# Performance work log

Hardware: AMD Instinct MI355X
Metric: run time of the kernel (lower is better)

## Reference

```python
import jax, jax.numpy as jnp
import numpy as np

N, R, T = 40000, 2000, 500000   # node_size, rel_size, triple_size
D, DEPTH, PROXY_N = 128, 2, 64  # node_F, depth, proxy rows
DC = D * (DEPTH + 1)            # 384


def _unique_edges(rng, n_rows, n_cols, n_edges):
    # sorted, duplicate-free edge list -> matches torch.sparse coalesce() ordering
    keys = np.unique(rng.integers(0, n_rows * n_cols, size=int(n_edges * 1.05), dtype=np.int64))[:n_edges]
    assert keys.shape[0] == n_edges
    return np.stack([keys // n_cols, keys % n_cols], axis=1)


def _init_emb(key, r, c):
    w = jax.random.normal(key, (r, c), dtype=jnp.float32)
    return w / jnp.maximum(jnp.linalg.norm(w, axis=1, keepdims=True), 1e-12)


def setup_inputs() -> dict:
    rng = np.random.default_rng(0)
    adj = jnp.asarray(_unique_edges(rng, N, N, T))                    # [T,2] (src, dst)
    idx = jnp.stack([jnp.arange(T), jnp.asarray(rng.integers(0, R, T, dtype=np.int64))], axis=1)  # [T,2]
    val = jnp.ones((T,), jnp.float32)
    ent_m = jnp.asarray(_unique_edges(rng, N, N, T))
    rel_m = jnp.asarray(_unique_edges(rng, N, R, T))
    ks = jax.random.split(jax.random.key(0), 12)
    return {
        "ent_emb": _init_emb(ks[0], N, D),
        "rel_emb": _init_emb(ks[1], R, D),
        "e_gate": _init_emb(ks[2], DC, DC),
        "e_proxy": _init_emb(ks[3], PROXY_N, DC),
        "e_bias": _init_emb(ks[4], 1, DC),
        "e_attn": jnp.stack([_init_emb(ks[5], D, 1), _init_emb(ks[6], D, 1)]),
        "r_gate": _init_emb(ks[7], DC, DC),
        "r_proxy": _init_emb(ks[8], PROXY_N, DC),
        "r_bias": _init_emb(ks[9], 1, DC),
        "r_attn": jnp.stack([_init_emb(ks[10], D, 1), _init_emb(ks[11], D, 1)]),
        "val_input": val,
        "adj_input": adj,
        "index_input": idx,
        "ent_matrix": ent_m,
        "rel_matrix": rel_m,
    }


def _l2(x):
    return x / jnp.maximum(jnp.linalg.norm(x, axis=-1, keepdims=True), 1e-12)


def _seg_softmax(v, seg, n):
    m = jax.ops.segment_max(v, seg, num_segments=n)
    e = jnp.exp(v - m[seg])
    s = jax.ops.segment_sum(e, seg, num_segments=n)
    return e / s[seg]


def _adj_agg(edges, emb, n_rows):
    # torch.sparse.softmax over rows of an all-ones adjacency, then sparse @ emb
    rows, cols = edges[:, 0], edges[:, 1]
    w = _seg_softmax(jnp.zeros(edges.shape[0], emb.dtype), rows, n_rows)
    return jax.ops.segment_sum(w[:, None] * emb[cols], rows, num_segments=n_rows)


def _graph_attention(features, rel_emb, edges, sp_idx, sp_val, attn, gate_k, proxy, bias):
    n = features.shape[0]
    t = sp_val.shape[0]
    feats = jnp.tanh(features)
    outs = [feats]
    for l in range(DEPTH):
        # sparse (T,R) @ rel_emb -> per-edge relation embedding, then L2 normalize
        rels_sum = _l2(jax.ops.segment_sum(sp_val[:, None] * rel_emb[sp_idx[:, 1]], sp_idx[:, 0], num_segments=t))
        neighs = feats[edges[:, 1]]                                   # [T,D]
        neighs = neighs - 2.0 * jnp.sum(neighs * rels_sum, axis=1, keepdims=True) * rels_sum  # Householder reflection
        att = _seg_softmax((rels_sum @ attn[l])[:, 0], edges[:, 0], n)  # sparse row softmax
        feats = jnp.tanh(jax.ops.segment_sum(neighs * att[:, None], edges[:, 0], num_segments=n))
        outs.append(feats)
    outputs = jnp.concatenate(outs, axis=1)                           # [N, DC]
    pa = jax.nn.softmax(_l2(outputs) @ _l2(proxy).T, axis=-1)         # [N, 64]
    pf = outputs - pa @ proxy
    gate = jax.nn.sigmoid(pf @ gate_k + bias)
    return gate * outputs + (1.0 - gate) * pf


def reference(ent_emb, rel_emb, e_gate, e_proxy, e_bias, e_attn, r_gate, r_proxy, r_bias, r_attn, val_input, adj_input, index_input, ent_matrix, rel_matrix):
    ent_feature = _adj_agg(ent_matrix, ent_emb, N)                    # [N,D]
    rel_feature = _adj_agg(rel_matrix, rel_emb, N)                    # [N,D]
    out_e = _graph_attention(ent_feature, rel_emb, adj_input, index_input, val_input, e_attn, e_gate, e_proxy, e_bias)
    out_r = _graph_attention(rel_feature, rel_emb, adj_input, index_input, val_input, r_attn, r_gate, r_proxy, r_bias)
    # dropout_rate = 0.0 -> identity
    return jnp.concatenate([out_e, out_r], axis=-1)                   # [N, 2*DC]
```

## Files before the change

### kernel.cpp

```cpp
#include <hip/hip_runtime.h>
#include <hip/hip_fp16.h>


typedef __attribute__((ext_vector_type(4))) float f32x4;
typedef _Float16 h16x2 __attribute__((ext_vector_type(2)));
typedef _Float16 f16x8 __attribute__((ext_vector_type(8)));
typedef float f32x16 __attribute__((ext_vector_type(16)));

__device__ __forceinline__ float wave_sum(float v) {
#pragma unroll
  for (int o = 32; o > 0; o >>= 1) v += __shfl_xor(v, o, 64);
  return v;
}
__device__ __forceinline__ float wave_max(float v) {
#pragma unroll
  for (int o = 32; o > 0; o >>= 1) v = fmaxf(v, __shfl_xor(v, o, 64));
  return v;
}
__device__ __forceinline__ unsigned pkhalf2(float a, float b) {
  __half2 h = __floats2half2_rn(a, b);
  return __builtin_bit_cast(unsigned, h);
}
__device__ __forceinline__ float bcf(unsigned u) {
  return __builtin_bit_cast(float, u);
}
__device__ __forceinline__ unsigned short f2h(float x) {
  return __builtin_bit_cast(unsigned short, (_Float16)x);
}
__device__ __forceinline__ float h2f(unsigned short h) {
  return (float)__builtin_bit_cast(_Float16, h);
}
__device__ __forceinline__ float tanh_fast(float x) {
  float t = __expf(-2.f * fabsf(x));
  float y = (1.f - t) / (1.f + t);
  return copysignf(y, x);
}
__device__ __forceinline__ float fdot2u(unsigned a, unsigned b, float c) {
#if __has_builtin(__builtin_amdgcn_fdot2)
  return __builtin_amdgcn_fdot2(__builtin_bit_cast(h16x2, a),
                                __builtin_bit_cast(h16x2, b), c, false);
#else
  h16x2 x = __builtin_bit_cast(h16x2, a), y = __builtin_bit_cast(h16x2, b);
  return fmaf((float)x.x, (float)y.x, fmaf((float)x.y, (float)y.y, c));
#endif
}

__global__ void rowptr3_kernel(const int* __restrict__ e0,
                               const int* __restrict__ e1,
                               const int* __restrict__ e2, int T, int N,
                               int* __restrict__ p0, int* __restrict__ p1,
                               int* __restrict__ p2) {
  int tid = blockIdx.x * blockDim.x + threadIdx.x;
  int which = tid / (N + 1);
  int r = tid - which * (N + 1);
  if (which >= 3) return;
  const int* E = which == 0 ? e0 : (which == 1 ? e1 : e2);
  int* P = which == 0 ? p0 : (which == 1 ? p1 : p2);
  int lo = 0, hi = T;
  while (lo < hi) {
    int mid = (lo + hi) >> 1;
    if (E[2 * mid] < r) lo = mid + 1; else hi = mid;
  }
  P[r] = lo;
}

__global__ void relprep_kernel(const float* __restrict__ rel_emb,
                               const float* __restrict__ e_attn,
                               const float* __restrict__ r_attn, int R,
                               float* __restrict__ srel,
                               unsigned* __restrict__ rnorm,
                               unsigned* __restrict__ rel16) {
  int r = blockIdx.x * 4 + (threadIdx.x >> 6);
  int lane = threadIdx.x & 63;
  if (r >= R) return;
  float2 v  = *(const float2*)(rel_emb + (size_t)r * 128 + 2 * lane);
  float2 a0 = *(const float2*)(e_attn + 2 * lane);
  float2 a1 = *(const float2*)(e_attn + 128 + 2 * lane);
  float2 b0 = *(const float2*)(r_attn + 2 * lane);
  float2 b1 = *(const float2*)(r_attn + 128 + 2 * lane);
  float n  = wave_sum(v.x * v.x + v.y * v.y);
  float d0 = wave_sum(v.x * a0.x + v.y * a0.y);
  float d1 = wave_sum(v.x * a1.x + v.y * a1.y);
  float d2 = wave_sum(v.x * b0.x + v.y * b0.y);
  float d3 = wave_sum(v.x * b1.x + v.y * b1.y);
  float inv = 1.f / fmaxf(sqrtf(n), 1e-12f);
  rnorm[(size_t)r * 64 + lane] = pkhalf2(v.x * inv, v.y * inv);
  rel16[(size_t)r * 64 + lane] = pkhalf2(v.x, v.y);
  if (lane == 0) {
    srel[r]          = d0 * inv;
    srel[R + r]      = d1 * inv;
    srel[2 * R + r]  = d2 * inv;
    srel[3 * R + r]  = d3 * inv;
  }
}

__global__ void pack_f16_kernel(const float* __restrict__ src,
                                unsigned* __restrict__ dst, int n2) {
  int i = blockIdx.x * blockDim.x + threadIdx.x;
  if (i >= n2) return;
  float2 v = *(const float2*)(src + 2 * (size_t)i);
  dst[i] = pkhalf2(v.x, v.y);
}

__global__ __launch_bounds__(256) void stats_kernel(
    const int* __restrict__ ptr, const int* __restrict__ idx,
    const float* __restrict__ srel, int R, float* __restrict__ stats, int N) {
  int r = blockIdx.x * 4 + (threadIdx.x >> 6);
  if (r >= N) return;
  int lane = threadIdx.x & 63;
  int beg = ptr[r], end = ptr[r + 1];
  const float* s0 = srel;
  const float* s1 = srel + R;
  const float* s2 = srel + 2 * R;
  const float* s3 = srel + 3 * R;
  float m0 = -INFINITY, m1 = -INFINITY, m2 = -INFINITY, m3 = -INFINITY;
  for (int e = beg + lane; e < end; e += 64) {
    int rel = idx[2 * e + 1];
    m0 = fmaxf(m0, s0[rel]); m1 = fmaxf(m1, s1[rel]);
    m2 = fmaxf(m2, s2[rel]); m3 = fmaxf(m3, s3[rel]);
  }
#pragma unroll
  for (int o = 32; o > 0; o >>= 1) {
    m0 = fmaxf(m0, __shfl_xor(m0, o, 64));
    m1 = fmaxf(m1, __shfl_xor(m1, o, 64));
    m2 = fmaxf(m2, __shfl_xor(m2, o, 64));
    m3 = fmaxf(m3, __shfl_xor(m3, o, 64));
  }
  float d0 = 0.f, d1 = 0.f, d2 = 0.f, d3 = 0.f;
  for (int e = beg + lane; e < end; e += 64) {
    int rel = idx[2 * e + 1];
    d0 += __expf(s0[rel] - m0); d1 += __expf(s1[rel] - m1);
    d2 += __expf(s2[rel] - m2); d3 += __expf(s3[rel] - m3);
  }
#pragma unroll
  for (int o = 32; o > 0; o >>= 1) {
    d0 += __shfl_xor(d0, o, 64); d1 += __shfl_xor(d1, o, 64);
    d2 += __shfl_xor(d2, o, 64); d3 += __shfl_xor(d3, o, 64);
  }
  if (lane == 0) {
    float4 a, b;
    a.x = m0; a.y = (d0 > 0.f) ? 1.f / d0 : 0.f;
    a.z = m1; a.w = (d1 > 0.f) ? 1.f / d1 : 0.f;
    b.x = m2; b.y = (d2 > 0.f) ? 1.f / d2 : 0.f;
    b.z = m3; b.w = (d3 > 0.f) ? 1.f / d3 : 0.f;
    *(float4*)(stats + (size_t)r * 8) = a;
    *(float4*)(stats + (size_t)r * 8 + 4) = b;
  }
}

__global__ void weight_kernel(const int* __restrict__ adj,
                              const int* __restrict__ idx,
                              const float* __restrict__ srel, int R,
                              const float* __restrict__ stats,
                              unsigned* __restrict__ pk,
                              uint2* __restrict__ wt0,
                              uint2* __restrict__ wt1, int T) {
  int e = blockIdx.x * blockDim.x + threadIdx.x;
  if (e >= T) return;
  int row = adj[2 * e];
  int col = adj[2 * e + 1];
  int rel = idx[2 * e + 1];
  float4 a = *(const float4*)(stats + (size_t)row * 8);
  float4 b = *(const float4*)(stats + (size_t)row * 8 + 4);
  float w0 = __expf(srel[rel] - a.x) * a.y;
  float w1 = __expf(srel[R + rel] - a.z) * a.w;
  float w2 = __expf(srel[2 * R + rel] - b.x) * b.y;
  float w3 = __expf(srel[3 * R + rel] - b.z) * b.w;
  pk[e] = (unsigned)col | ((unsigned)rel << 16);
  wt0[e] = make_uint2(__builtin_bit_cast(unsigned, w0),
                      __builtin_bit_cast(unsigned, w2));
  wt1[e] = make_uint2(__builtin_bit_cast(unsigned, w1),
                      __builtin_bit_cast(unsigned, w3));
}

__global__ __launch_bounds__(256) void agg_fused_kernel(
    const int* __restrict__ ptrE, const int* __restrict__ edgesE,
    const unsigned* __restrict__ ent16, const int* __restrict__ ptrR,
    const int* __restrict__ edgesR, const unsigned* __restrict__ rel16,
    unsigned* __restrict__ fout, int N) {
  int r = blockIdx.x * 4 + (threadIdx.x >> 6);
  if (r >= N) return;
  int lane = threadIdx.x & 63;
  int g = lane >> 4, q = lane & 15;

  float aE[8] = {0, 0, 0, 0, 0, 0, 0, 0};
  float aR[8] = {0, 0, 0, 0, 0, 0, 0, 0};

  auto addh = [&](uint4 u, float* a) {
    h16x2 h0 = __builtin_bit_cast(h16x2, u.x), h1 = __builtin_bit_cast(h16x2, u.y);
    h16x2 h2 = __builtin_bit_cast(h16x2, u.z), h3 = __builtin_bit_cast(h16x2, u.w);
    a[0] += (float)h0.x; a[1] += (float)h0.y;
    a[2] += (float)h1.x; a[3] += (float)h1.y;
    a[4] += (float)h2.x; a[5] += (float)h2.y;
    a[6] += (float)h3.x; a[7] += (float)h3.y;
  };

  int begE = ptrE[r], endE = ptrE[r + 1];
  for (int e0 = begE; e0 < endE; e0 += 8) {
    int eA = e0 + g, eB = e0 + 4 + g;
    if (eA < endE)
      addh(*(const uint4*)(ent16 + (size_t)edgesE[2 * eA + 1] * 64 + 4 * q), aE);
    if (eB < endE)
      addh(*(const uint4*)(ent16 + (size_t)edgesE[2 * eB + 1] * 64 + 4 * q), aE);
  }
  int begR = ptrR[r], endR = ptrR[r + 1];
  for (int e0 = begR; e0 < endR; e0 += 8) {
    int eA = e0 + g, eB = e0 + 4 + g;
    if (eA < endR)
      addh(*(const uint4*)(rel16 + (size_t)edgesR[2 * eA + 1] * 64 + 4 * q), aR);
    if (eB < endR)
      addh(*(const uint4*)(rel16 + (size_t)edgesR[2 * eB + 1] * 64 + 4 * q), aR);
  }
#pragma unroll
  for (int j = 0; j < 8; ++j) {
    aE[j] += __shfl_xor(aE[j], 16, 64); aE[j] += __shfl_xor(aE[j], 32, 64);
    aR[j] += __shfl_xor(aR[j], 16, 64); aR[j] += __shfl_xor(aR[j], 32, 64);
  }
  float sE = (endE > begE) ? 1.f / (float)(endE - begE) : 0.f;
  float sR = (endR > begR) ? 1.f / (float)(endR - begR) : 0.f;
  if (g == 0) {
    float t[8];
#pragma unroll
    for (int j = 0; j < 8; ++j) t[j] = tanh_fast(aE[j] * sE);
    uint4 u;
    u.x = pkhalf2(t[0], t[1]); u.y = pkhalf2(t[2], t[3]);
    u.z = pkhalf2(t[4], t[5]); u.w = pkhalf2(t[6], t[7]);
    *(uint4*)(fout + (size_t)r * 128 + 4 * q) = u;
  } else if (g == 1) {
    float t[8];
#pragma unroll
    for (int j = 0; j < 8; ++j) t[j] = tanh_fast(aR[j] * sR);
    uint4 u;
    u.x = pkhalf2(t[0], t[1]); u.y = pkhalf2(t[2], t[3]);
    u.z = pkhalf2(t[4], t[5]); u.w = pkhalf2(t[6], t[7]);
    *(uint4*)(fout + (size_t)r * 128 + 64 + 4 * q) = u;
  }
}

__global__ __launch_bounds__(256) void layer_rec_kernel(
    const int* __restrict__ ptr, const unsigned* __restrict__ pk,
    const uint2* __restrict__ wt, const unsigned* __restrict__ rnorm,
    const unsigned* __restrict__ fin, unsigned* __restrict__ foutE,
    unsigned* __restrict__ foutR, int fstride, int N) {
  int r = blockIdx.x * 4 + (threadIdx.x >> 6);
  if (r >= N) return;
  int lane = threadIdx.x & 63;
  int g = lane >> 4, q = lane & 15;
  int beg = ptr[r], end = ptr[r + 1];

  float aE[8] = {0, 0, 0, 0, 0, 0, 0, 0};
  float aR[8] = {0, 0, 0, 0, 0, 0, 0, 0};

  auto accum = [&](uint4 F, uint4 V, float w, float s, float* a) {
    h16x2 f0 = __builtin_bit_cast(h16x2, F.x), v0 = __builtin_bit_cast(h16x2, V.x);
    h16x2 f1 = __builtin_bit_cast(h16x2, F.y), v1 = __builtin_bit_cast(h16x2, V.y);
    h16x2 f2 = __builtin_bit_cast(h16x2, F.z), v2 = __builtin_bit_cast(h16x2, V.z);
    h16x2 f3 = __builtin_bit_cast(h16x2, F.w), v3 = __builtin_bit_cast(h16x2, V.w);
    a[0] = fmaf((float)f0.x, w, fmaf((float)v0.x, s, a[0]));
    a[1] = fmaf((float)f0.y, w, fmaf((float)v0.y, s, a[1]));
    a[2] = fmaf((float)f1.x, w, fmaf((float)v1.x, s, a[2]));
    a[3] = fmaf((float)f1.y, w, fmaf((float)v1.y, s, a[3]));
    a[4] = fmaf((float)f2.x, w, fmaf((float)v2.x, s, a[4]));
    a[5] = fmaf((float)f2.y, w, fmaf((float)v2.y, s, a[5]));
    a[6] = fmaf((float)f3.x, w, fmaf((float)v3.x, s, a[6]));
    a[7] = fmaf((float)f3.y, w, fmaf((float)v3.y, s, a[7]));
  };

  for (int e0 = beg; e0 < end; e0 += 8) {
    int eA = e0 + g, eB = e0 + 4 + g;
    bool actA = eA < end, actB = eB < end;
    unsigned pkA = actA ? pk[eA] : 0u;
    unsigned pkB = actB ? pk[eB] : 0u;
    uint2 wA = actA ? wt[eA] : make_uint2(0u, 0u);
    uint2 wB = actB ? wt[eB] : make_uint2(0u, 0u);
    int colA = (int)(pkA & 0xFFFFu), relA = (int)(pkA >> 16);
    int colB = (int)(pkB & 0xFFFFu), relB = (int)(pkB >> 16);
    float wAE = bcf(wA.x), wAR = bcf(wA.y);
    float wBE = bcf(wB.x), wBR = bcf(wB.y);

    const unsigned* fA = fin + (size_t)colA * 128;
    const unsigned* fB = fin + (size_t)colB * 128;
    uint4 EA = *(const uint4*)(fA + 4 * q);
    uint4 RA = *(const uint4*)(fA + 64 + 4 * q);
    uint4 VA = *(const uint4*)(rnorm + (size_t)relA * 64 + 4 * q);
    uint4 EB = *(const uint4*)(fB + 4 * q);
    uint4 RB = *(const uint4*)(fB + 64 + 4 * q);
    uint4 VB = *(const uint4*)(rnorm + (size_t)relB * 64 + 4 * q);

    float dAE = fdot2u(EA.w, VA.w, fdot2u(EA.z, VA.z,
                fdot2u(EA.y, VA.y, fdot2u(EA.x, VA.x, 0.f))));
    float dAR = fdot2u(RA.w, VA.w, fdot2u(RA.z, VA.z,
                fdot2u(RA.y, VA.y, fdot2u(RA.x, VA.x, 0.f))));
    float dBE = fdot2u(EB.w, VB.w, fdot2u(EB.z, VB.z,
                fdot2u(EB.y, VB.y, fdot2u(EB.x, VB.x, 0.f))));
    float dBR = fdot2u(RB.w, VB.w, fdot2u(RB.z, VB.z,
                fdot2u(RB.y, VB.y, fdot2u(RB.x, VB.x, 0.f))));
#pragma unroll
    for (int m = 1; m < 16; m <<= 1) {
      dAE += __shfl_xor(dAE, m, 64);
      dAR += __shfl_xor(dAR, m, 64);
      dBE += __shfl_xor(dBE, m, 64);
      dBR += __shfl_xor(dBR, m, 64);
    }
    float sAE = -2.f * wAE * dAE, sAR = -2.f * wAR * dAR;
    float sBE = -2.f * wBE * dBE, sBR = -2.f * wBR * dBR;
    accum(EA, VA, wAE, sAE, aE);
    accum(RA, VA, wAR, sAR, aR);
    accum(EB, VB, wBE, sBE, aE);
    accum(RB, VB, wBR, sBR, aR);
  }

#pragma unroll
  for (int j = 0; j < 8; ++j) {
    aE[j] += __shfl_xor(aE[j], 16, 64); aE[j] += __shfl_xor(aE[j], 32, 64);
    aR[j] += __shfl_xor(aR[j], 16, 64); aR[j] += __shfl_xor(aR[j], 32, 64);
  }
  if (g == 0) {
    float t[8];
#pragma unroll
    for (int j = 0; j < 8; ++j) t[j] = tanh_fast(aE[j]);
    uint4 u;
    u.x = pkhalf2(t[0], t[1]); u.y = pkhalf2(t[2], t[3]);
    u.z = pkhalf2(t[4], t[5]); u.w = pkhalf2(t[6], t[7]);
    *(uint4*)(foutE + (size_t)r * fstride + 4 * q) = u;
  } else if (g == 1) {
    float t[8];
#pragma unroll
    for (int j = 0; j < 8; ++j) t[j] = tanh_fast(aR[j]);
    uint4 u;
    u.x = pkhalf2(t[0], t[1]); u.y = pkhalf2(t[2], t[3]);
    u.z = pkhalf2(t[4], t[5]); u.w = pkhalf2(t[6], t[7]);
    *(uint4*)(foutR + (size_t)r * fstride + 4 * q) = u;
  }
}

__device__ __forceinline__ void pack_one32(const float* __restrict__ src,
                                           unsigned short* __restrict__ dst,
                                           int NT, int srcld, int mode, int f,
                                           int lane) {
  int kt = f / NT, nt = f % NT;
  int kbase = 16 * kt + 8 * (lane >> 5);
  int n = 32 * nt + (lane & 31);
  unsigned short tmp[8];
#pragma unroll
  for (int j = 0; j < 8; ++j) {
    int k = kbase + j;
    float v = (mode == 0) ? src[(size_t)k * srcld + n] : src[(size_t)n * srcld + k];
    tmp[j] = f2h(v);
  }
  *(uint4*)(dst + ((size_t)f * 64 + lane) * 8) = *(uint4*)tmp;
}
__global__ void pack_all_kernel(const float* eP, const float* eG,
                                const float* rP, const float* rG,
                                unsigned short* b1e, unsigned short* b2e,
                                unsigned short* b3e, unsigned short* b1r,
                                unsigned short* b2r, unsigned short* b3r) {
  int f = blockIdx.x * 4 + (threadIdx.x >> 6);
  int lane = threadIdx.x & 63;
  if (f < 48)       pack_one32(eP, b1e, 2, 384, 1, f, lane);
  else if (f < 96)  pack_one32(eP, b2e, 12, 384, 0, f - 48, lane);
  else if (f < 384) pack_one32(eG, b3e, 12, 384, 0, f - 96, lane);
  else if (f < 432) pack_one32(rP, b1r, 2, 384, 1, f - 384, lane);
  else if (f < 480) pack_one32(rP, b2r, 12, 384, 0, f - 432, lane);
  else if (f < 768) pack_one32(rG, b3r, 12, 384, 0, f - 480, lane);
}

__global__ __launch_bounds__(256) void final_fused_kernel(
    const unsigned* __restrict__ f0, const unsigned* __restrict__ f1,
    const unsigned* __restrict__ outu,
    const unsigned short* __restrict__ B1e, const unsigned short* __restrict__ B2e,
    const unsigned short* __restrict__ B3e, const unsigned short* __restrict__ B1r,
    const unsigned short* __restrict__ B2r, const unsigned short* __restrict__ B3r,
    const float* __restrict__ biasE, const float* __restrict__ biasR,
    float* __restrict__ gout) {
  __shared__ __align__(16) unsigned sOutH[32][204];
  __shared__ __align__(16) float sPa[32][68];
  __shared__ __align__(16) unsigned short sPaH[32][72];
  __shared__ float sInv[32];
  unsigned short* sOutHs = (unsigned short*)&sOutH[0][0];

  const int side = blockIdx.x & 1;
  const int row0 = (blockIdx.x >> 1) * 32;
  const int plane = side ? 64 : 0;
  const unsigned* f2 = outu + (side ? 704 : 0);
  const unsigned short* B1 = side ? B1r : B1e;
  const unsigned short* B2 = side ? B2r : B2e;
  const unsigned short* B3 = side ? B3r : B3e;
  const float* bias = side ? biasR : biasE;
  const int coloff = side ? 384 : 0;

  const int t = threadIdx.x;
  const int w = t >> 6, lane = t & 63;
  const int l31 = lane & 31, l5 = lane >> 5;

  {
    int rloc = t >> 3;
    int c0 = t & 7;
    int rg = row0 + rloc;
    float ss = 0.f;
#pragma unroll
    for (int i = 0; i < 6; ++i) {
      int c = c0 + 8 * i;
      int buf = c >> 4, j = c & 15;
      const unsigned* src;
      if (buf == 0)      src = f0 + (size_t)rg * 128 + plane + 4 * j;
      else if (buf == 1) src = f1 + (size_t)rg * 128 + plane + 4 * j;
      else               src = f2 + (size_t)rg * 768 + 4 * j;
      uint4 u = *(const uint4*)src;
      *(uint4*)&sOutH[rloc][c * 4] = u;
      ss = fdot2u(u.x, u.x, fdot2u(u.y, u.y,
           fdot2u(u.z, u.z, fdot2u(u.w, u.w, ss))));
    }
    ss += __shfl_xor(ss, 1, 64);
    ss += __shfl_xor(ss, 2, 64);
    ss += __shfl_xor(ss, 4, 64);
    if (c0 == 0) sInv[rloc] = 1.f / fmaxf(sqrtf(ss), 1e-12f);
  }
  __syncthreads();

  if (w < 2) {
    int ct = w;
    f32x16 acc = {0.f, 0.f, 0.f, 0.f, 0.f, 0.f, 0.f, 0.f,
                  0.f, 0.f, 0.f, 0.f, 0.f, 0.f, 0.f, 0.f};
#pragma unroll
    for (int kt = 0; kt < 24; ++kt) {
      f16x8 a = __builtin_bit_cast(
          f16x8, *(const uint4*)&sOutH[l31][8 * kt + 4 * l5]);
      f16x8 b = *(const f16x8*)(B1 + ((size_t)(kt * 2 + ct) * 64 + lane) * 8);
      acc = __builtin_amdgcn_mfma_f32_32x32x16_f16(a, b, acc, 0, 0, 0);
    }
#pragma unroll
    for (int reg = 0; reg < 16; ++reg) {
      int row = (reg & 3) + 8 * (reg >> 2) + 4 * l5;
      sPa[row][ct * 32 + l31] = acc[reg] * sInv[row];
    }
  }
  __syncthreads();

  for (int rr = 8 * w; rr < 8 * w + 8; ++rr) {
    float v = sPa[rr][lane];
    float mx = wave_max(v);
    float e = __expf(v - mx);
    float s = wave_sum(e);
    sPaH[rr][lane] = f2h(e / s);
  }
  __syncthreads();

  const int ntb = 3 * w;
  unsigned outv[3][8];
  {
    f32x16 acc2[3];
#pragma unroll
    for (int s = 0; s < 3; ++s)
#pragma unroll
      for (int i = 0; i < 16; ++i) acc2[s][i] = 0.f;
#pragma unroll
    for (int kt = 0; kt < 4; ++kt) {
      f16x8 a = __builtin_bit_cast(
          f16x8, *(const uint4*)&sPaH[l31][16 * kt + 8 * l5]);
#pragma unroll
      for (int s = 0; s < 3; ++s) {
        f16x8 b = *(const f16x8*)(B2 + ((size_t)(kt * 12 + ntb + s) * 64 + lane) * 8);
        acc2[s] = __builtin_amdgcn_mfma_f32_32x32x16_f16(a, b, acc2[s], 0, 0, 0);
      }
    }
#pragma unroll
    for (int s = 0; s < 3; ++s) {
      int col = 32 * (ntb + s) + l31;
#pragma unroll
      for (int p = 0; p < 8; ++p) {
        int ra = ((2 * p) & 3) + 8 * (p >> 1) + 4 * l5;
        unsigned short u0 = sOutHs[ra * 408 + col];
        unsigned short u1 = sOutHs[(ra + 1) * 408 + col];
        outv[s][p] = (unsigned)u0 | ((unsigned)u1 << 16);
        float pf0 = h2f(u0) - acc2[s][2 * p];
        float pf1 = h2f(u1) - acc2[s][2 * p + 1];
        sOutHs[ra * 408 + col] = f2h(pf0);
        sOutHs[(ra + 1) * 408 + col] = f2h(pf1);
      }
    }
  }
  __syncthreads();

  f32x16 acc3[3];
#pragma unroll
  for (int s = 0; s < 3; ++s)
#pragma unroll
    for (int i = 0; i < 16; ++i) acc3[s][i] = 0.f;
#pragma unroll
  for (int kt = 0; kt < 24; ++kt) {
    f16x8 a = __builtin_bit_cast(
        f16x8, *(const uint4*)&sOutH[l31][8 * kt + 4 * l5]);
#pragma unroll
    for (int s = 0; s < 3; ++s) {
      f16x8 b = *(const f16x8*)(B3 + ((size_t)(kt * 12 + ntb + s) * 64 + lane) * 8);
      acc3[s] = __builtin_amdgcn_mfma_f32_32x32x16_f16(a, b, acc3[s], 0, 0, 0);
    }
  }

#pragma unroll
  for (int s = 0; s < 3; ++s) {
    int col = 32 * (ntb + s) + l31;
    float bv = bias[col];
#pragma unroll
    for (int p = 0; p < 8; ++p) {
      int ra = ((2 * p) & 3) + 8 * (p >> 1) + 4 * l5;
      float g0 = 1.f / (1.f + __expf(-(acc3[s][2 * p] + bv)));
      float g1 = 1.f / (1.f + __expf(-(acc3[s][2 * p + 1] + bv)));
      float pf0 = h2f(sOutHs[ra * 408 + col]);
      float pf1 = h2f(sOutHs[(ra + 1) * 408 + col]);
      unsigned ov = outv[s][p];
      float o0 = h2f((unsigned short)(ov & 0xffffu));
      float o1 = h2f((unsigned short)(ov >> 16));
      gout[(size_t)(row0 + ra) * 768 + coloff + col] = g0 * o0 + (1.f - g0) * pf0;
      gout[(size_t)(row0 + ra + 1) * 768 + coloff + col] =
          g1 * o1 + (1.f - g1) * pf1;
    }
  }
}

extern "C" void kernel_launch(void* const* d_in, const int* in_sizes, int n_in,
                              void* d_out, int out_size, void* d_ws,
                              size_t ws_size, hipStream_t stream) {
  (void)n_in; (void)out_size; (void)ws_size;
  const float* ent_emb = (const float*)d_in[0];
  const float* rel_emb = (const float*)d_in[1];
  const float* e_gate  = (const float*)d_in[2];
  const float* e_proxy = (const float*)d_in[3];
  const float* e_bias  = (const float*)d_in[4];
  const float* e_attn  = (const float*)d_in[5];
  const float* r_gate  = (const float*)d_in[6];
  const float* r_proxy = (const float*)d_in[7];
  const float* r_bias  = (const float*)d_in[8];
  const float* r_attn  = (const float*)d_in[9];
  const int* adj   = (const int*)d_in[11];
  const int* idx   = (const int*)d_in[12];
  const int* ent_m = (const int*)d_in[13];
  const int* rel_m = (const int*)d_in[14];
  const int N = in_sizes[0] / 128;
  const int R = in_sizes[1] / 128;
  const int T = in_sizes[10];
  float* out = (float*)d_out;

  char* w = (char*)d_ws;
  size_t used = 0;
  auto alloc = [&](size_t bytes) {
    void* p = (void*)(w + used);
    used += (bytes + 255) & ~(size_t)255;
    return p;
  };
  int* ptr_adj  = (int*)alloc((size_t)(N + 1) * sizeof(int));
  int* ptr_ent  = (int*)alloc((size_t)(N + 1) * sizeof(int));
  int* ptr_rel  = (int*)alloc((size_t)(N + 1) * sizeof(int));
  float* srel   = (float*)alloc((size_t)4 * R * sizeof(float));
  unsigned short* b1e = (unsigned short*)alloc(48 * 1024);
  unsigned short* b2e = (unsigned short*)alloc(48 * 1024);
  unsigned short* b3e = (unsigned short*)alloc(288 * 1024);
  unsigned short* b1r = (unsigned short*)alloc(48 * 1024);
  unsigned short* b2r = (unsigned short*)alloc(48 * 1024);
  unsigned short* b3r = (unsigned short*)alloc(288 * 1024);
  unsigned* rnorm = (unsigned*)alloc((size_t)R * 64 * 4);
  unsigned* rel16 = (unsigned*)alloc((size_t)R * 64 * 4);
  unsigned* ent16 = (unsigned*)alloc((size_t)N * 64 * 4);
  unsigned* fsrc0 = (unsigned*)alloc((size_t)N * 128 * 4);
  unsigned* fsrc1 = (unsigned*)alloc((size_t)N * 128 * 4);
  float* stats = (float*)alloc((size_t)N * 8 * sizeof(float));
  unsigned* pk = (unsigned*)alloc((size_t)T * 4);
  uint2* wt0 = (uint2*)alloc((size_t)T * 8);
  uint2* wt1 = (uint2*)alloc((size_t)T * 8);

  dim3 b256(256);
  rowptr3_kernel<<<(3 * (N + 1) + 255) / 256, b256, 0, stream>>>(
      adj, ent_m, rel_m, T, N, ptr_adj, ptr_ent, ptr_rel);
  relprep_kernel<<<(R + 3) / 4, b256, 0, stream>>>(rel_emb, e_attn, r_attn, R,
                                                   srel, rnorm, rel16);
  pack_f16_kernel<<<(N * 64 + 255) / 256, b256, 0, stream>>>(ent_emb, ent16,
                                                             N * 64);
  pack_all_kernel<<<192, b256, 0, stream>>>(e_proxy, e_gate, r_proxy, r_gate,
                                            b1e, b2e, b3e, b1r, b2r, b3r);

  int grow = (N + 3) / 4;
  stats_kernel<<<grow, b256, 0, stream>>>(ptr_adj, idx, srel, R, stats, N);
  weight_kernel<<<(T + 255) / 256, b256, 0, stream>>>(adj, idx, srel, R, stats,
                                                      pk, wt0, wt1, T);
  agg_fused_kernel<<<grow, b256, 0, stream>>>(ptr_ent, ent_m, ent16, ptr_rel,
                                              rel_m, rel16, fsrc0, N);
  unsigned* outu = (unsigned*)out;
  layer_rec_kernel<<<grow, b256, 0, stream>>>(ptr_adj, pk, wt0, rnorm, fsrc0,
                                              fsrc1, fsrc1 + 64, 128, N);
  layer_rec_kernel<<<grow, b256, 0, stream>>>(ptr_adj, pk, wt1, rnorm, fsrc1,
                                              outu, outu + 704, 768, N);

  int fblocks = 2 * ((N + 31) / 32);
  final_fused_kernel<<<fblocks, b256, 0, stream>>>(
      fsrc0, fsrc1, outu, b1e, b2e, b3e, b1r, b2r, b3r, e_bias, r_bias, out);
}
```

Measured before the change: 293.7 us.

## Precompute per-relation exp scores and drop per-edge weight materialization

```diff
diff --git a/kernel.cpp b/kernel.cpp
--- a/kernel.cpp
+++ b/kernel.cpp
@@ -20,9 +20,6 @@
 __device__ __forceinline__ unsigned pkhalf2(float a, float b) {
   __half2 h = __floats2half2_rn(a, b);
   return __builtin_bit_cast(unsigned, h);
-}
-__device__ __forceinline__ float bcf(unsigned u) {
-  return __builtin_bit_cast(float, u);
 }
 __device__ __forceinline__ unsigned short f2h(float x) {
   return __builtin_bit_cast(unsigned short, (_Float16)x);
@@ -43,6 +40,10 @@
   h16x2 x = __builtin_bit_cast(h16x2, a), y = __builtin_bit_cast(h16x2, b);
   return fmaf((float)x.x, (float)y.x, fmaf((float)x.y, (float)y.y, c));
 #endif
+}
+__device__ __forceinline__ float dot8(uint4 a, uint4 b) {
+  return fdot2u(a.w, b.w, fdot2u(a.z, b.z, fdot2u(a.y, b.y,
+         fdot2u(a.x, b.x, 0.f))));
 }
 
 __global__ void rowptr3_kernel(const int* __restrict__ e0,
@@ -67,7 +68,7 @@
 __global__ void relprep_kernel(const float* __restrict__ rel_emb,
                                const float* __restrict__ e_attn,
                                const float* __restrict__ r_attn, int R,
-                               float* __restrict__ srel,
+                               float4* __restrict__ expS4,
                                unsigned* __restrict__ rnorm,
                                unsigned* __restrict__ rel16) {
   int r = blockIdx.x * 4 + (threadIdx.x >> 6);
@@ -87,10 +88,8 @@
   rnorm[(size_t)r * 64 + lane] = pkhalf2(v.x * inv, v.y * inv);
   rel16[(size_t)r * 64 + lane] = pkhalf2(v.x, v.y);
   if (lane == 0) {
-    srel[r]          = d0 * inv;
-    srel[R + r]      = d1 * inv;
-    srel[2 * R + r]  = d2 * inv;
-    srel[3 * R + r]  = d3 * inv;
+    expS4[r] = make_float4(__expf(d0 * inv), __expf(d1 * inv),
+                           __expf(d2 * inv), __expf(d3 * inv));
   }
 }
 
@@ -102,35 +101,25 @@
   dst[i] = pkhalf2(v.x, v.y);
 }
 
-__global__ __launch_bounds__(256) void stats_kernel(
-    const int* __restrict__ ptr, const int* __restrict__ idx,
-    const float* __restrict__ srel, int R, float* __restrict__ stats, int N) {
+__global__ void pack_edges_kernel(const int* __restrict__ adj,
+                                  const int* __restrict__ idx,
+                                  unsigned* __restrict__ pk, int T) {
+  int e = blockIdx.x * blockDim.x + threadIdx.x;
+  if (e >= T) return;
+  pk[e] = (unsigned)adj[2 * e + 1] | ((unsigned)idx[2 * e + 1] << 16);
+}
+
+__global__ __launch_bounds__(256) void stats4_kernel(
+    const int* __restrict__ ptr, const unsigned* __restrict__ pk,
+    const float4* __restrict__ expS4, float4* __restrict__ inv4, int N) {
   int r = blockIdx.x * 4 + (threadIdx.x >> 6);
   if (r >= N) return;
   int lane = threadIdx.x & 63;
   int beg = ptr[r], end = ptr[r + 1];
-  const float* s0 = srel;
-  const float* s1 = srel + R;
-  const float* s2 = srel + 2 * R;
-  const float* s3 = srel + 3 * R;
-  float m0 = -INFINITY, m1 = -INFINITY, m2 = -INFINITY, m3 = -INFINITY;
-  for (int e = beg + lane; e < end; e += 64) {
-    int rel = idx[2 * e + 1];
-    m0 = fmaxf(m0, s0[rel]); m1 = fmaxf(m1, s1[rel]);
-    m2 = fmaxf(m2, s2[rel]); m3 = fmaxf(m3, s3[rel]);
-  }
-#pragma unroll
-  for (int o = 32; o > 0; o >>= 1) {
-    m0 = fmaxf(m0, __shfl_xor(m0, o, 64));
-    m1 = fmaxf(m1, __shfl_xor(m1, o, 64));
-    m2 = fmaxf(m2, __shfl_xor(m2, o, 64));
-    m3 = fmaxf(m3, __shfl_xor(m3, o, 64));
-  }
   float d0 = 0.f, d1 = 0.f, d2 = 0.f, d3 = 0.f;
   for (int e = beg + lane; e < end; e += 64) {
-    int rel = idx[2 * e + 1];
-    d0 += __expf(s0[rel] - m0); d1 += __expf(s1[rel] - m1);
-    d2 += __expf(s2[rel] - m2); d3 += __expf(s3[rel] - m3);
+    float4 es = expS4[pk[e] >> 16];
+    d0 += es.x; d1 += es.y; d2 += es.z; d3 += es.w;
   }
 #pragma unroll
   for (int o = 32; o > 0; o >>= 1) {
@@ -138,39 +127,11 @@
     d2 += __shfl_xor(d2, o, 64); d3 += __shfl_xor(d3, o, 64);
   }
   if (lane == 0) {
-    float4 a, b;
-    a.x = m0; a.y = (d0 > 0.f) ? 1.f / d0 : 0.f;
-    a.z = m1; a.w = (d1 > 0.f) ? 1.f / d1 : 0.f;
-    b.x = m2; b.y = (d2 > 0.f) ? 1.f / d2 : 0.f;
-    b.z = m3; b.w = (d3 > 0.f) ? 1.f / d3 : 0.f;
-    *(float4*)(stats + (size_t)r * 8) = a;
-    *(float4*)(stats + (size_t)r * 8 + 4) = b;
-  }
-}
-
-__global__ void weight_kernel(const int* __restrict__ adj,
-                              const int* __restrict__ idx,
-                              const float* __restrict__ srel, int R,
-                              const float* __restrict__ stats,
-                              unsigned* __restrict__ pk,
-                              uint2* __restrict__ wt0,
-                              uint2* __restrict__ wt1, int T) {
-  int e = blockIdx.x * blockDim.x + threadIdx.x;
-  if (e >= T) return;
-  int row = adj[2 * e];
-  int col = adj[2 * e + 1];
-  int rel = idx[2 * e + 1];
-  float4 a = *(const float4*)(stats + (size_t)row * 8);
-  float4 b = *(const float4*)(stats + (size_t)row * 8 + 4);
-  float w0 = __expf(srel[rel] - a.x) * a.y;
-  float w1 = __expf(srel[R + rel] - a.z) * a.w;
-  float w2 = __expf(srel[2 * R + rel] - b.x) * b.y;
-  float w3 = __expf(srel[3 * R + rel] - b.z) * b.w;
-  pk[e] = (unsigned)col | ((unsigned)rel << 16);
-  wt0[e] = make_uint2(__builtin_bit_cast(unsigned, w0),
-                      __builtin_bit_cast(unsigned, w2));
-  wt1[e] = make_uint2(__builtin_bit_cast(unsigned, w1),
-                      __builtin_bit_cast(unsigned, w3));
+    inv4[r] = make_float4(d0 > 0.f ? 1.f / d0 : 0.f,
+                          d1 > 0.f ? 1.f / d1 : 0.f,
+                          d2 > 0.f ? 1.f / d2 : 0.f,
+                          d3 > 0.f ? 1.f / d3 : 0.f);
+  }
 }
 
 __global__ __launch_bounds__(256) void agg_fused_kernel(
@@ -196,20 +157,28 @@
   };
 
   int begE = ptrE[r], endE = ptrE[r + 1];
-  for (int e0 = begE; e0 < endE; e0 += 8) {
-    int eA = e0 + g, eB = e0 + 4 + g;
+  for (int e0 = begE; e0 < endE; e0 += 16) {
+    int eA = e0 + g, eB = eA + 4, eC = eA + 8, eD = eA + 12;
     if (eA < endE)
       addh(*(const uint4*)(ent16 + (size_t)edgesE[2 * eA + 1] * 64 + 4 * q), aE);
     if (eB < endE)
       addh(*(const uint4*)(ent16 + (size_t)edgesE[2 * eB + 1] * 64 + 4 * q), aE);
+    if (eC < endE)
+      addh(*(const uint4*)(ent16 + (size_t)edgesE[2 * eC + 1] * 64 + 4 * q), aE);
+    if (eD < endE)
+      addh(*(const uint4*)(ent16 + (size_t)edgesE[2 * eD + 1] * 64 + 4 * q), aE);
   }
   int begR = ptrR[r], endR = ptrR[r + 1];
-  for (int e0 = begR; e0 < endR; e0 += 8) {
-    int eA = e0 + g, eB = e0 + 4 + g;
+  for (int e0 = begR; e0 < endR; e0 += 16) {
+    int eA = e0 + g, eB = eA + 4, eC = eA + 8, eD = eA + 12;
     if (eA < endR)
       addh(*(const uint4*)(rel16 + (size_t)edgesR[2 * eA + 1] * 64 + 4 * q), aR);
     if (eB < endR)
       addh(*(const uint4*)(rel16 + (size_t)edgesR[2 * eB + 1] * 64 + 4 * q), aR);
+    if (eC < endR)
+      addh(*(const uint4*)(rel16 + (size_t)edgesR[2 * eC + 1] * 64 + 4 * q), aR);
+    if (eD < endR)
+      addh(*(const uint4*)(rel16 + (size_t)edgesR[2 * eD + 1] * 64 + 4 * q), aR);
   }
 #pragma unroll
   for (int j = 0; j < 8; ++j) {
@@ -239,14 +208,18 @@
 
 __global__ __launch_bounds__(256) void layer_rec_kernel(
     const int* __restrict__ ptr, const unsigned* __restrict__ pk,
-    const uint2* __restrict__ wt, const unsigned* __restrict__ rnorm,
-    const unsigned* __restrict__ fin, unsigned* __restrict__ foutE,
-    unsigned* __restrict__ foutR, int fstride, int N) {
+    const float4* __restrict__ expS4, const float4* __restrict__ inv4,
+    const unsigned* __restrict__ rnorm, const unsigned* __restrict__ fin,
+    unsigned* __restrict__ foutE, unsigned* __restrict__ foutR, int fstride,
+    int N, int lay) {
   int r = blockIdx.x * 4 + (threadIdx.x >> 6);
   if (r >= N) return;
   int lane = threadIdx.x & 63;
   int g = lane >> 4, q = lane & 15;
   int beg = ptr[r], end = ptr[r + 1];
+  float4 iv = inv4[r];
+  float ivE = lay ? iv.y : iv.x;
+  float ivR = lay ? iv.w : iv.z;
 
   float aE[8] = {0, 0, 0, 0, 0, 0, 0, 0};
   float aR[8] = {0, 0, 0, 0, 0, 0, 0, 0};
@@ -266,48 +239,62 @@
     a[7] = fmaf((float)f3.y, w, fmaf((float)v3.y, s, a[7]));
   };
 
-  for (int e0 = beg; e0 < end; e0 += 8) {
-    int eA = e0 + g, eB = e0 + 4 + g;
-    bool actA = eA < end, actB = eB < end;
-    unsigned pkA = actA ? pk[eA] : 0u;
-    unsigned pkB = actB ? pk[eB] : 0u;
-    uint2 wA = actA ? wt[eA] : make_uint2(0u, 0u);
-    uint2 wB = actB ? wt[eB] : make_uint2(0u, 0u);
-    int colA = (int)(pkA & 0xFFFFu), relA = (int)(pkA >> 16);
-    int colB = (int)(pkB & 0xFFFFu), relB = (int)(pkB >> 16);
-    float wAE = bcf(wA.x), wAR = bcf(wA.y);
-    float wBE = bcf(wB.x), wBR = bcf(wB.y);
+  for (int e0 = beg; e0 < end; e0 += 16) {
+    int eA = e0 + g, eB = eA + 4, eC = eA + 8, eD = eA + 12;
+    bool cA = eA < end, cB = eB < end, cC = eC < end, cD = eD < end;
+    unsigned pA = cA ? pk[eA] : 0u, pB = cB ? pk[eB] : 0u;
+    unsigned pC = cC ? pk[eC] : 0u, pD = cD ? pk[eD] : 0u;
+    int colA = (int)(pA & 0xFFFFu), relA = (int)(pA >> 16);
+    int colB = (int)(pB & 0xFFFFu), relB = (int)(pB >> 16);
+    int colC = (int)(pC & 0xFFFFu), relC = (int)(pC >> 16);
+    int colD = (int)(pD & 0xFFFFu), relD = (int)(pD >> 16);
 
     const unsigned* fA = fin + (size_t)colA * 128;
     const unsigned* fB = fin + (size_t)colB * 128;
+    const unsigned* fC = fin + (size_t)colC * 128;
+    const unsigned* fD = fin + (size_t)colD * 128;
     uint4 EA = *(const uint4*)(fA + 4 * q);
     uint4 RA = *(const uint4*)(fA + 64 + 4 * q);
     uint4 VA = *(const uint4*)(rnorm + (size_t)relA * 64 + 4 * q);
     uint4 EB = *(const uint4*)(fB + 4 * q);
     uint4 RB = *(const uint4*)(fB + 64 + 4 * q);
     uint4 VB = *(const uint4*)(rnorm + (size_t)relB * 64 + 4 * q);
-
-    float dAE = fdot2u(EA.w, VA.w, fdot2u(EA.z, VA.z,
-                fdot2u(EA.y, VA.y, fdot2u(EA.x, VA.x, 0.f))));
-    float dAR = fdot2u(RA.w, VA.w, fdot2u(RA.z, VA.z,
-                fdot2u(RA.y, VA.y, fdot2u(RA.x, VA.x, 0.f))));
-    float dBE = fdot2u(EB.w, VB.w, fdot2u(EB.z, VB.z,
-                fdot2u(EB.y, VB.y, fdot2u(EB.x, VB.x, 0.f))));
-    float dBR = fdot2u(RB.w, VB.w, fdot2u(RB.z, VB.z,
-                fdot2u(RB.y, VB.y, fdot2u(RB.x, VB.x, 0.f))));
+    uint4 EC = *(const uint4*)(fC + 4 * q);
+    uint4 RC = *(const uint4*)(fC + 64 + 4 * q);
+    uint4 VC = *(const uint4*)(rnorm + (size_t)relC * 64 + 4 * q);
+    uint4 ED = *(const uint4*)(fD + 4 * q);
+    uint4 RD = *(const uint4*)(fD + 64 + 4 * q);
+    uint4 VD = *(const uint4*)(rnorm + (size_t)relD * 64 + 4 * q);
+
+    float dAE = dot8(EA, VA), dAR = dot8(RA, VA);
+    float dBE = dot8(EB, VB), dBR = dot8(RB, VB);
+    float dCE = dot8(EC, VC), dCR = dot8(RC, VC);
+    float dDE = dot8(ED, VD), dDR = dot8(RD, VD);
 #pragma unroll
     for (int m = 1; m < 16; m <<= 1) {
-      dAE += __shfl_xor(dAE, m, 64);
-      dAR += __shfl_xor(dAR, m, 64);
-      dBE += __shfl_xor(dBE, m, 64);
-      dBR += __shfl_xor(dBR, m, 64);
-    }
-    float sAE = -2.f * wAE * dAE, sAR = -2.f * wAR * dAR;
-    float sBE = -2.f * wBE * dBE, sBR = -2.f * wBR * dBR;
-    accum(EA, VA, wAE, sAE, aE);
-    accum(RA, VA, wAR, sAR, aR);
-    accum(EB, VB, wBE, sBE, aE);
-    accum(RB, VB, wBR, sBR, aR);
+      dAE += __shfl_xor(dAE, m, 64); dAR += __shfl_xor(dAR, m, 64);
+      dBE += __shfl_xor(dBE, m, 64); dBR += __shfl_xor(dBR, m, 64);
+      dCE += __shfl_xor(dCE, m, 64); dCR += __shfl_xor(dCR, m, 64);
+      dDE += __shfl_xor(dDE, m, 64); dDR += __shfl_xor(dDR, m, 64);
+    }
+
+    float4 esA = cA ? expS4[relA] : make_float4(0, 0, 0, 0);
+    float4 esB = cB ? expS4[relB] : make_float4(0, 0, 0, 0);
+    float4 esC = cC ? expS4[relC] : make_float4(0, 0, 0, 0);
+    float4 esD = cD ? expS4[relD] : make_float4(0, 0, 0, 0);
+    float wAE = (lay ? esA.y : esA.x) * ivE, wAR = (lay ? esA.w : esA.z) * ivR;
+    float wBE = (lay ? esB.y : esB.x) * ivE, wBR = (lay ? esB.w : esB.z) * ivR;
+    float wCE = (lay ? esC.y : esC.x) * ivE, wCR = (lay ? esC.w : esC.z) * ivR;
+    float wDE = (lay ? esD.y : esD.x) * ivE, wDR = (lay ? esD.w : esD.z) * ivR;
+
+    accum(EA, VA, wAE, -2.f * wAE * dAE, aE);
+    accum(RA, VA, wAR, -2.f * wAR * dAR, aR);
+    accum(EB, VB, wBE, -2.f * wBE * dBE, aE);
+    accum(RB, VB, wBR, -2.f * wBR * dBR, aR);
+    accum(EC, VC, wCE, -2.f * wCE * dCE, aE);
+    accum(RC, VC, wCR, -2.f * wCR * dCR, aR);
+    accum(ED, VD, wDE, -2.f * wDE * dDE, aE);
+    accum(RD, VD, wDR, -2.f * wDR * dDR, aR);
   }
 
 #pragma unroll
@@ -552,7 +539,6 @@
   int* ptr_adj  = (int*)alloc((size_t)(N + 1) * sizeof(int));
   int* ptr_ent  = (int*)alloc((size_t)(N + 1) * sizeof(int));
   int* ptr_rel  = (int*)alloc((size_t)(N + 1) * sizeof(int));
-  float* srel   = (float*)alloc((size_t)4 * R * sizeof(float));
   unsigned short* b1e = (unsigned short*)alloc(48 * 1024);
   unsigned short* b2e = (unsigned short*)alloc(48 * 1024);
   unsigned short* b3e = (unsigned short*)alloc(288 * 1024);
@@ -564,32 +550,32 @@
   unsigned* ent16 = (unsigned*)alloc((size_t)N * 64 * 4);
   unsigned* fsrc0 = (unsigned*)alloc((size_t)N * 128 * 4);
   unsigned* fsrc1 = (unsigned*)alloc((size_t)N * 128 * 4);
-  float* stats = (float*)alloc((size_t)N * 8 * sizeof(float));
+  float4* expS4 = (float4*)alloc((size_t)R * 16);
+  float4* inv4  = (float4*)alloc((size_t)N * 16);
   unsigned* pk = (unsigned*)alloc((size_t)T * 4);
-  uint2* wt0 = (uint2*)alloc((size_t)T * 8);
-  uint2* wt1 = (uint2*)alloc((size_t)T * 8);
 
   dim3 b256(256);
   rowptr3_kernel<<<(3 * (N + 1) + 255) / 256, b256, 0, stream>>>(
       adj, ent_m, rel_m, T, N, ptr_adj, ptr_ent, ptr_rel);
   relprep_kernel<<<(R + 3) / 4, b256, 0, stream>>>(rel_emb, e_attn, r_attn, R,
-                                                   srel, rnorm, rel16);
+                                                   expS4, rnorm, rel16);
   pack_f16_kernel<<<(N * 64 + 255) / 256, b256, 0, stream>>>(ent_emb, ent16,
                                                              N * 64);
+  pack_edges_kernel<<<(T + 255) / 256, b256, 0, stream>>>(adj, idx, pk, T);
   pack_all_kernel<<<192, b256, 0, stream>>>(e_proxy, e_gate, r_proxy, r_gate,
                                             b1e, b2e, b3e, b1r, b2r, b3r);
 
   int grow = (N + 3) / 4;
-  stats_kernel<<<grow, b256, 0, stream>>>(ptr_adj, idx, srel, R, stats, N);
-  weight_kernel<<<(T + 255) / 256, b256, 0, stream>>>(adj, idx, srel, R, stats,
-                                                      pk, wt0, wt1, T);
+  stats4_kernel<<<grow, b256, 0, stream>>>(ptr_adj, pk, expS4, inv4, N);
   agg_fused_kernel<<<grow, b256, 0, stream>>>(ptr_ent, ent_m, ent16, ptr_rel,
                                               rel_m, rel16, fsrc0, N);
   unsigned* outu = (unsigned*)out;
-  layer_rec_kernel<<<grow, b256, 0, stream>>>(ptr_adj, pk, wt0, rnorm, fsrc0,
-                                              fsrc1, fsrc1 + 64, 128, N);
-  layer_rec_kernel<<<grow, b256, 0, stream>>>(ptr_adj, pk, wt1, rnorm, fsrc1,
-                                              outu, outu + 704, 768, N);
+  layer_rec_kernel<<<grow, b256, 0, stream>>>(ptr_adj, pk, expS4, inv4, rnorm,
+                                              fsrc0, fsrc1, fsrc1 + 64, 128,
+                                              N, 0);
+  layer_rec_kernel<<<grow, b256, 0, stream>>>(ptr_adj, pk, expS4, inv4, rnorm,
+                                              fsrc1, outu, outu + 704, 768,
+                                              N, 1);
 
   int fblocks = 2 * ((N + 31) / 32);
   final_fused_kernel<<<fblocks, b256, 0, stream>>>(
```

Result: slower. 312.2 us (+6.3%).
